# Performance work log

Hardware: AMD Instinct MI355X
Metric: run time of the kernel (lower is better)

## Reference

```python
import jax, jax.numpy as jnp
import numpy as np

N_NODES = 100000
N_EDGES = 1200000
D_FEAT = 64


def setup_inputs() -> dict:
    key = jax.random.key(0)
    k1, k2, k3 = jax.random.split(key, 3)
    x = jax.random.normal(k1, (N_NODES, D_FEAT), dtype=jnp.float32)
    edge_index = jax.random.randint(k2, (2, N_EDGES), 0, N_NODES, dtype=jnp.int64)
    edge_weight = jax.random.uniform(k3, (N_EDGES, 1), dtype=jnp.float32)
    return {"x": x, "edge_index": edge_index, "edge_weight": edge_weight}


def reference(x, edge_index, edge_weight):
    # flow = source_to_target: j = edge_index[0] (source), i = edge_index[1] (target)
    src, dst = edge_index[0], edge_index[1]
    # message: x_j  (gather along node_dim=-2)
    msg = x[src]                       # [E, D]
    # aggregate: scatter-'sum' with edge_weight scaling
    msg = msg * edge_weight            # [E, D]
    out = jax.ops.segment_sum(msg, dst, num_segments=N_NODES)  # [N, D]
    # update: identity
    return out
```

## Files before the change

### kernel.cpp

```cpp
#include <hip/hip_runtime.h>
#include <hip/hip_bf16.h>


constexpr int D_FEAT        = 64;
constexpr int BIN_SHIFT     = 7;
constexpr int NODES_PER_BIN = 1 << BIN_SHIFT;
constexpr int NBINS_MAX     = 1024;
constexpr int BIN_CAP       = 2048;
constexpr int EPB           = 4096;
constexpr int OVF_CAP       = 32768;
constexpr int NKEYS         = 1024;

__device__ __forceinline__ int wave_incl_scan(int v, int lane) {
    #pragma unroll
    for (int d = 1; d < 64; d <<= 1) {
        int t = __shfl_up(v, d);
        if (lane >= d) v += t;
    }
    return v;
}

__device__ __forceinline__ unsigned short f32_to_bf16_rn(float f) {
    unsigned int u = __float_as_uint(f);
    u += 0x7FFFu + ((u >> 16) & 1u);
    return (unsigned short)(u >> 16);
}

__global__ __launch_bounds__(1024) void mp_partition(
    const int* __restrict__ src, const int* __restrict__ dst,
    const float* __restrict__ w, const float* __restrict__ x,
    ushort* __restrict__ xb, int n4,
    int*  __restrict__ gcnt,
    int2* __restrict__ payload,
    int*  __restrict__ ovf_cnt, int4* __restrict__ ovf,
    int n_edges, int nbins)
{
    __shared__ int cnt[NBINS_MAX];
    __shared__ int start[NBINS_MAX];
    __shared__ int cur[NBINS_MAX];
    __shared__ int gbase[NBINS_MAX];
    __shared__ unsigned short binof[EPB];
    __shared__ int2 sorted[EPB];
    __shared__ int wsum[16];

    const int t    = threadIdx.x;
    const int lane = t & 63;
    const int wid  = t >> 6;
    const int base = blockIdx.x * EPB;
    const int nblk = min(EPB, n_edges - base);

    if (t < NBINS_MAX) cnt[t] = 0;

    const int i4 = (base >> 2) + t;
    const bool have = (i4 * 4 < n_edges);
    int4 d4 = make_int4(0, 0, 0, 0);
    if (have) d4 = reinterpret_cast<const int4*>(dst)[i4];

    for (int i = blockIdx.x * 1024 + t; i < n4; i += gridDim.x * 1024) {
        const float4 v = reinterpret_cast<const float4*>(x)[i];
        ushort4 o;
        o.x = f32_to_bf16_rn(v.x);
        o.y = f32_to_bf16_rn(v.y);
        o.z = f32_to_bf16_rn(v.z);
        o.w = f32_to_bf16_rn(v.w);
        reinterpret_cast<ushort4*>(xb)[i] = o;
    }
    __syncthreads();

    if (have) {
        atomicAdd(&cnt[d4.x >> BIN_SHIFT], 1);
        atomicAdd(&cnt[d4.y >> BIN_SHIFT], 1);
        atomicAdd(&cnt[d4.z >> BIN_SHIFT], 1);
        atomicAdd(&cnt[d4.w >> BIN_SHIFT], 1);
    }
    __syncthreads();

    const int c = (t < nbins) ? cnt[t] : 0;
    const int incl = wave_incl_scan(c, lane);
    if (lane == 63) wsum[wid] = incl;
    __syncthreads();
    int woff = 0;
    #pragma unroll
    for (int k = 0; k < 16; ++k) woff += (k < wid) ? wsum[k] : 0;
    const int excl = woff + incl - c;
    if (t < nbins) {
        start[t] = excl;
        cur[t]   = excl;
        if (c > 0) gbase[t] = atomicAdd(&gcnt[t], c);
    }
    __syncthreads();

    if (have) {
        const int4   s4 = reinterpret_cast<const int4*>(src)[i4];
        const float4 w4 = reinterpret_cast<const float4*>(w)[i4];
        const int   dd[4] = {d4.x, d4.y, d4.z, d4.w};
        const int   ss[4] = {s4.x, s4.y, s4.z, s4.w};
        const float ww[4] = {w4.x, w4.y, w4.z, w4.w};
        #pragma unroll
        for (int j = 0; j < 4; ++j) {
            const int b   = dd[j] >> BIN_SHIFT;
            const int low = dd[j] & (NODES_PER_BIN - 1);
            const int p   = atomicAdd(&cur[b], 1);
            sorted[p] = make_int2((low << 20) | ss[j], __float_as_int(ww[j]));
            binof[p]  = (unsigned short)b;
        }
    }
    __syncthreads();

    #pragma unroll
    for (int k = 0; k < EPB / 1024; ++k) {
        const int i = k * 1024 + t;
        if (i >= nblk) break;
        const int b    = binof[i];
        const int idx  = i - start[b];
        const int gpos = gbase[b] + idx;
        const int2 e   = sorted[i];
        if (gpos < BIN_CAP) {
            payload[(size_t)b * BIN_CAP + gpos] = e;
        } else {
            const int op = atomicAdd(ovf_cnt, 1);
            if (op < OVF_CAP)
                ovf[op] = make_int4((b << BIN_SHIFT) + (e.x >> 20),
                                    e.x & 0xFFFFF, e.y, 0);
        }
    }
}


#define ACC8(XV, WW) do {                                          \
    a0 = fmaf(__uint_as_float((XV).x << 16),         (WW), a0);    \
    a1 = fmaf(__uint_as_float((XV).x & 0xFFFF0000u), (WW), a1);    \
    a2 = fmaf(__uint_as_float((XV).y << 16),         (WW), a2);    \
    a3 = fmaf(__uint_as_float((XV).y & 0xFFFF0000u), (WW), a3);    \
    a4 = fmaf(__uint_as_float((XV).z << 16),         (WW), a4);    \
    a5 = fmaf(__uint_as_float((XV).z & 0xFFFF0000u), (WW), a5);    \
    a6 = fmaf(__uint_as_float((XV).w << 16),         (WW), a6);    \
    a7 = fmaf(__uint_as_float((XV).w & 0xFFFF0000u), (WW), a7);    \
} while (0)

__global__ __launch_bounds__(512) void mp_bin_gather(
    const ushort* __restrict__ xb,
    const float*  __restrict__ x,
    const int*  __restrict__ gcnt,
    const int2* __restrict__ payload,
    const int*  __restrict__ ovf_cnt, const int4* __restrict__ ovf,
    float* __restrict__ out, int n_nodes)
{
    __shared__ int2 sraw[BIN_CAP];
    __shared__ int2 sedge[BIN_CAP];
    __shared__ int ncnt[NKEYS];
    __shared__ int nstart[NKEYS + 1];
    __shared__ int ncur[NKEYS];
    __shared__ int wsum[8];

    const int b    = blockIdx.x;
    const int t    = threadIdx.x;
    const int wid  = t >> 6;
    const int lane = t & 63;
    const int sub  = lane >> 3;
    const int fq   = lane & 7;
    const int fg   = fq * 8;

    const int m = min(gcnt[b], BIN_CAP);
    const int2* pl = payload + (size_t)b * BIN_CAP;

    for (int i = t; i < NKEYS; i += 512) ncnt[i] = 0;
    __syncthreads();

    for (int i = t; i < m; i += 512) {
        const int2 e = pl[i];
        sraw[i] = e;
        const int key = ((e.x >> 20) << 3) | ((e.x & 0xFFFFF) >> 14);
        atomicAdd(&ncnt[key], 1);
    }
    __syncthreads();

    {
        const int base0 = wid * 128;
        const int c0 = ncnt[base0 + lane];
        const int c1 = ncnt[base0 + 64 + lane];
        const int s0_ = wave_incl_scan(c0, lane);
        const int t0  = __shfl(s0_, 63);
        const int s1_ = wave_incl_scan(c1, lane) + t0;
        if (lane == 63) wsum[wid] = s1_;
        __syncthreads();
        int cpre = 0;
        #pragma unroll
        for (int k = 0; k < 8; ++k) cpre += (k < wid) ? wsum[k] : 0;
        const int e0 = cpre + s0_ - c0;
        const int e1 = cpre + s1_ - c1;
        nstart[base0 + lane]      = e0;  ncur[base0 + lane]      = e0;
        nstart[base0 + 64 + lane] = e1;  ncur[base0 + 64 + lane] = e1;
        if (t == 511) nstart[NKEYS] = cpre + s1_;
    }
    __syncthreads();

    for (int i = t; i < m; i += 512) {
        const int2 e = sraw[i];
        const int key = ((e.x >> 20) << 3) | ((e.x & 0xFFFFF) >> 14);
        const int p  = atomicAdd(&ncur[key], 1);
        sedge[p] = e;
    }
    __syncthreads();

    const int novf = *ovf_cnt;

    #define XROW(SRC) (*reinterpret_cast<const uint4*>(xb + (size_t)(SRC) * D_FEAT + fg))

    #pragma unroll
    for (int nb = 0; nb < 16; nb += 8) {
        const int n    = wid * 16 + nb + sub;
        const int node = (b << BIN_SHIFT) + n;
        const int s0 = nstart[n << 3];
        const int s1 = nstart[(n + 1) << 3];

        float a0 = 0.f, a1 = 0.f, a2 = 0.f, a3 = 0.f;
        float a4 = 0.f, a5 = 0.f, a6 = 0.f, a7 = 0.f;

        int e = s0;
        for (; e + 4 <= s1; e += 4) {
            const int2 pA = sedge[e];
            const int2 pB = sedge[e + 1];
            const int2 pC = sedge[e + 2];
            const int2 pD = sedge[e + 3];
            const uint4 xA = XROW(pA.x & 0xFFFFF);
            const uint4 xB = XROW(pB.x & 0xFFFFF);
            const uint4 xC = XROW(pC.x & 0xFFFFF);
            const uint4 xD = XROW(pD.x & 0xFFFFF);
            const float wA = __int_as_float(pA.y);
            const float wB = __int_as_float(pB.y);
            const float wC = __int_as_float(pC.y);
            const float wD = __int_as_float(pD.y);
            ACC8(xA, wA);
            ACC8(xB, wB);
            ACC8(xC, wC);
            ACC8(xD, wD);
        }
        if (e + 2 <= s1) {
            const int2 pA = sedge[e];
            const int2 pB = sedge[e + 1];
            const uint4 xA = XROW(pA.x & 0xFFFFF);
            const uint4 xB = XROW(pB.x & 0xFFFFF);
            const float wA = __int_as_float(pA.y);
            const float wB = __int_as_float(pB.y);
            ACC8(xA, wA);
            ACC8(xB, wB);
            e += 2;
        }
        if (e < s1) {
            const int2 p = sedge[e];
            const uint4 xv = XROW(p.x & 0xFFFFF);
            const float ww = __int_as_float(p.y);
            ACC8(xv, ww);
        }

        if (node < n_nodes) {
            if (novf > 0) {
                const int lim = min(novf, OVF_CAP);
                for (int j = 0; j < lim; ++j) {
                    const int4 o = ovf[j];
                    if (o.x == node) {
                        const float* xr = x + (size_t)o.y * D_FEAT + fg;
                        const float ww = __int_as_float(o.z);
                        a0 = fmaf(xr[0], ww, a0); a1 = fmaf(xr[1], ww, a1);
                        a2 = fmaf(xr[2], ww, a2); a3 = fmaf(xr[3], ww, a3);
                        a4 = fmaf(xr[4], ww, a4); a5 = fmaf(xr[5], ww, a5);
                        a6 = fmaf(xr[6], ww, a6); a7 = fmaf(xr[7], ww, a7);
                    }
                }
            }
            float* orow = out + (size_t)node * D_FEAT + fg;
            *reinterpret_cast<float4*>(orow)     = make_float4(a0, a1, a2, a3);
            *reinterpret_cast<float4*>(orow + 4) = make_float4(a4, a5, a6, a7);
        }
    }
    #undef XROW
}

__global__ __launch_bounds__(256) void mp_scatter_atomic(
    const float* __restrict__ x, const int* __restrict__ src,
    const int* __restrict__ dst, const float* __restrict__ w,
    float* __restrict__ out, int n_edges)
{
    const int gtid = blockIdx.x * blockDim.x + threadIdx.x;
    const int edge = gtid >> 6;
    const int lane = threadIdx.x & 63;
    if (edge >= n_edges) return;
    const int s = src[edge];
    const int d = dst[edge];
    const float ww = w[edge];
    atomicAdd(&out[(size_t)d * D_FEAT + lane], x[(size_t)s * D_FEAT + lane] * ww);
}

extern "C" void kernel_launch(void* const* d_in, const int* in_sizes, int n_in,
                              void* d_out, int out_size, void* d_ws, size_t ws_size,
                              hipStream_t stream)
{
    const float* x          = (const float*)d_in[0];
    const int*   edge_index = (const int*)d_in[1];
    const float* w          = (const float*)d_in[2];
    float*       out        = (float*)d_out;

    const int n_edges = in_sizes[1] / 2;
    const int n_nodes = in_sizes[0] / D_FEAT;
    const int* src = edge_index;
    const int* dst = edge_index + n_edges;

    const int nbins = (n_nodes + NODES_PER_BIN - 1) >> BIN_SHIFT;

    int*    gcnt    = (int*)d_ws;
    int*    ovf_cnt = gcnt + NBINS_MAX;
    int4*   ovf     = (int4*)(gcnt + NBINS_MAX + 64);
    int2*   payload = (int2*)(ovf + OVF_CAP);
    ushort* xb      = (ushort*)(payload + (size_t)nbins * BIN_CAP);
    const size_t need = (size_t)(NBINS_MAX + 64) * 4 + (size_t)OVF_CAP * 16
                      + (size_t)nbins * BIN_CAP * 8
                      + (size_t)n_nodes * D_FEAT * 2;

    const bool ok = (ws_size >= need) && (nbins <= NBINS_MAX) && ((n_edges & 3) == 0)
                 && ((n_nodes * D_FEAT) % 4 == 0) && (n_nodes <= 131072);

    if (ok) {
        hipMemsetAsync(gcnt, 0, (size_t)(NBINS_MAX + 64) * 4, stream);
        const int n4 = n_nodes * D_FEAT / 4;
        const int g1 = (n_edges + EPB - 1) / EPB;
        mp_partition<<<g1, 1024, 0, stream>>>(src, dst, w, x, xb, n4,
                                              gcnt, payload, ovf_cnt, ovf,
                                              n_edges, nbins);
        mp_bin_gather<<<nbins, 512, 0, stream>>>(xb, x, gcnt, payload,
                                                 ovf_cnt, ovf, out, n_nodes);
        return;
    }

    hipMemsetAsync(d_out, 0, (size_t)out_size * sizeof(float), stream);
    const int grid = (int)(((size_t)n_edges * 64 + 255) / 256);
    mp_scatter_atomic<<<grid, 256, 0, stream>>>(x, src, dst, w, out, n_edges);
}
```

Before: 126.0 us.

## Halve bin size to 64 nodes and drop the sub-key sort in gather

Bins shrink from 128 to 64 destination nodes, which doubles the bin count to 1563 and halves per-bin capacity. The partition kernel gets a two-element-per-thread scan over 2048 bins. The gather kernel runs with 256 threads and sorts edges by destination node only, dropping the 8-way source sub-key (source locality) ordering. The goal is more, smaller gather blocks for better occupancy and load balance, plus less sort work. In exchange, the partition kernel does more global atomics per block, and the lost source locality may hurt cache reuse.

```diff
diff --git a/kernel.cpp b/kernel.cpp
--- a/kernel.cpp
+++ b/kernel.cpp
@@ -3,13 +3,12 @@
 
 
 constexpr int D_FEAT        = 64;
-constexpr int BIN_SHIFT     = 7;
+constexpr int BIN_SHIFT     = 6;
 constexpr int NODES_PER_BIN = 1 << BIN_SHIFT;
-constexpr int NBINS_MAX     = 1024;
-constexpr int BIN_CAP       = 2048;
+constexpr int NBINS_MAX     = 2048;
+constexpr int BIN_CAP       = 1024;
 constexpr int EPB           = 4096;
 constexpr int OVF_CAP       = 32768;
-constexpr int NKEYS         = 1024;
 
 __device__ __forceinline__ int wave_incl_scan(int v, int lane) {
     #pragma unroll
@@ -49,7 +48,8 @@
     const int base = blockIdx.x * EPB;
     const int nblk = min(EPB, n_edges - base);
 
-    if (t < NBINS_MAX) cnt[t] = 0;
+    cnt[t] = 0;
+    cnt[t + 1024] = 0;
 
     const int i4 = (base >> 2) + t;
     const bool have = (i4 * 4 < n_edges);
@@ -75,18 +75,28 @@
     }
     __syncthreads();
 
-    const int c = (t < nbins) ? cnt[t] : 0;
-    const int incl = wave_incl_scan(c, lane);
-    if (lane == 63) wsum[wid] = incl;
-    __syncthreads();
-    int woff = 0;
-    #pragma unroll
-    for (int k = 0; k < 16; ++k) woff += (k < wid) ? wsum[k] : 0;
-    const int excl = woff + incl - c;
-    if (t < nbins) {
-        start[t] = excl;
-        cur[t]   = excl;
-        if (c > 0) gbase[t] = atomicAdd(&gcnt[t], c);
+    {
+        const int base0 = wid * 128;
+        const int c0 = cnt[base0 + lane];
+        const int c1 = cnt[base0 + 64 + lane];
+        const int s0_ = wave_incl_scan(c0, lane);
+        const int t0  = __shfl(s0_, 63);
+        const int s1_ = wave_incl_scan(c1, lane) + t0;
+        if (lane == 63) wsum[wid] = s1_;
+
+        for (int k = t; k < nbins; k += 1024) {
+            const int c = cnt[k];
+            if (c > 0) gbase[k] = atomicAdd(&gcnt[k], c);
+        }
+        __syncthreads();
+
+        int cpre = 0;
+        #pragma unroll
+        for (int k = 0; k < 16; ++k) cpre += (k < wid) ? wsum[k] : 0;
+        const int e0 = cpre + s0_ - c0;
+        const int e1 = cpre + s1_ - c1;
+        start[base0 + lane]      = e0;  cur[base0 + lane]      = e0;
+        start[base0 + 64 + lane] = e1;  cur[base0 + 64 + lane] = e1;
     }
     __syncthreads();
 
@@ -138,7 +148,7 @@
     a7 = fmaf(__uint_as_float((XV).w & 0xFFFF0000u), (WW), a7);    \
 } while (0)
 
-__global__ __launch_bounds__(512) void mp_bin_gather(
+__global__ __launch_bounds__(256) void mp_bin_gather(
     const ushort* __restrict__ xb,
     const float*  __restrict__ x,
     const int*  __restrict__ gcnt,
@@ -148,10 +158,9 @@
 {
     __shared__ int2 sraw[BIN_CAP];
     __shared__ int2 sedge[BIN_CAP];
-    __shared__ int ncnt[NKEYS];
-    __shared__ int nstart[NKEYS + 1];
-    __shared__ int ncur[NKEYS];
-    __shared__ int wsum[8];
+    __shared__ int ncnt[NODES_PER_BIN];
+    __shared__ int nstart[NODES_PER_BIN + 1];
+    __shared__ int ncur[NODES_PER_BIN];
 
     const int b    = blockIdx.x;
     const int t    = threadIdx.x;
@@ -164,41 +173,28 @@
     const int m = min(gcnt[b], BIN_CAP);
     const int2* pl = payload + (size_t)b * BIN_CAP;
 
-    for (int i = t; i < NKEYS; i += 512) ncnt[i] = 0;
-    __syncthreads();
-
-    for (int i = t; i < m; i += 512) {
+    if (t < NODES_PER_BIN) ncnt[t] = 0;
+    __syncthreads();
+
+    for (int i = t; i < m; i += 256) {
         const int2 e = pl[i];
         sraw[i] = e;
-        const int key = ((e.x >> 20) << 3) | ((e.x & 0xFFFFF) >> 14);
-        atomicAdd(&ncnt[key], 1);
-    }
-    __syncthreads();
-
-    {
-        const int base0 = wid * 128;
-        const int c0 = ncnt[base0 + lane];
-        const int c1 = ncnt[base0 + 64 + lane];
-        const int s0_ = wave_incl_scan(c0, lane);
-        const int t0  = __shfl(s0_, 63);
-        const int s1_ = wave_incl_scan(c1, lane) + t0;
-        if (lane == 63) wsum[wid] = s1_;
-        __syncthreads();
-        int cpre = 0;
-        #pragma unroll
-        for (int k = 0; k < 8; ++k) cpre += (k < wid) ? wsum[k] : 0;
-        const int e0 = cpre + s0_ - c0;
-        const int e1 = cpre + s1_ - c1;
-        nstart[base0 + lane]      = e0;  ncur[base0 + lane]      = e0;
-        nstart[base0 + 64 + lane] = e1;  ncur[base0 + 64 + lane] = e1;
-        if (t == 511) nstart[NKEYS] = cpre + s1_;
-    }
-    __syncthreads();
-
-    for (int i = t; i < m; i += 512) {
+        atomicAdd(&ncnt[e.x >> 20], 1);
+    }
+    __syncthreads();
+
+    if (t < 64) {
+        const int c0 = ncnt[t];
+        const int s0_ = wave_incl_scan(c0, t);
+        nstart[t] = s0_ - c0;
+        ncur[t]   = s0_ - c0;
+        if (t == 63) nstart[64] = s0_;
+    }
+    __syncthreads();
+
+    for (int i = t; i < m; i += 256) {
         const int2 e = sraw[i];
-        const int key = ((e.x >> 20) << 3) | ((e.x & 0xFFFFF) >> 14);
-        const int p  = atomicAdd(&ncur[key], 1);
+        const int p  = atomicAdd(&ncur[e.x >> 20], 1);
         sedge[p] = e;
     }
     __syncthreads();
@@ -211,8 +207,8 @@
     for (int nb = 0; nb < 16; nb += 8) {
         const int n    = wid * 16 + nb + sub;
         const int node = (b << BIN_SHIFT) + n;
-        const int s0 = nstart[n << 3];
-        const int s1 = nstart[(n + 1) << 3];
+        const int s0 = nstart[n];
+        const int s1 = nstart[n + 1];
 
         float a0 = 0.f, a1 = 0.f, a2 = 0.f, a3 = 0.f;
         float a4 = 0.f, a5 = 0.f, a6 = 0.f, a7 = 0.f;
@@ -327,7 +323,7 @@
         mp_partition<<<g1, 1024, 0, stream>>>(src, dst, w, x, xb, n4,
                                               gcnt, payload, ovf_cnt, ovf,
                                               n_edges, nbins);
-        mp_bin_gather<<<nbins, 512, 0, stream>>>(xb, x, gcnt, payload,
+        mp_bin_gather<<<nbins, 256, 0, stream>>>(xb, x, gcnt, payload,
                                                  ovf_cnt, ovf, out, n_nodes);
         return;
     }
```

After: 125.8 us. About the same (-0.1%).

## Fuse partition and bin-gather into one persistent cooperative kernel

Applied to the files above, without the earlier changes.

Replaces the memset, partition kernel and bin-gather kernel with a single cooperative persistent kernel that zeroes its counters, partitions edge chunks through an atomic work queue, converts x to bf16, then uses a grid sync before gathering per-bin. It also simplifies the per-bin sort to key on node only (128 keys instead of 1024 node/source sub-keys) and halves edges per chunk. The aim is to remove launch overhead and the tail between the two phases. In exchange it pays for grid-wide syncs and limits parallelism to the resident-block count. Dropping the source sub-key may also reduce locality in the x row gathers.

```diff
diff --git a/kernel.cpp b/kernel.cpp
--- a/kernel.cpp
+++ b/kernel.cpp
@@ -1,5 +1,8 @@
 #include <hip/hip_runtime.h>
+#include <hip/hip_cooperative_groups.h>
 #include <hip/hip_bf16.h>
+
+namespace cg = cooperative_groups;
 
 
 constexpr int D_FEAT        = 64;
@@ -7,9 +10,9 @@
 constexpr int NODES_PER_BIN = 1 << BIN_SHIFT;
 constexpr int NBINS_MAX     = 1024;
 constexpr int BIN_CAP       = 2048;
-constexpr int EPB           = 4096;
+constexpr int EPB           = 2048;
 constexpr int OVF_CAP       = 32768;
-constexpr int NKEYS         = 1024;
+constexpr int CONV_TILE     = 2048;
 
 __device__ __forceinline__ int wave_incl_scan(int v, int lane) {
     #pragma unroll
@@ -26,106 +29,23 @@
     return (unsigned short)(u >> 16);
 }
 
-__global__ __launch_bounds__(1024) void mp_partition(
-    const int* __restrict__ src, const int* __restrict__ dst,
-    const float* __restrict__ w, const float* __restrict__ x,
-    ushort* __restrict__ xb, int n4,
-    int*  __restrict__ gcnt,
-    int2* __restrict__ payload,
-    int*  __restrict__ ovf_cnt, int4* __restrict__ ovf,
-    int n_edges, int nbins)
-{
-    __shared__ int cnt[NBINS_MAX];
-    __shared__ int start[NBINS_MAX];
-    __shared__ int cur[NBINS_MAX];
-    __shared__ int gbase[NBINS_MAX];
-    __shared__ unsigned short binof[EPB];
-    __shared__ int2 sorted[EPB];
-    __shared__ int wsum[16];
-
-    const int t    = threadIdx.x;
-    const int lane = t & 63;
-    const int wid  = t >> 6;
-    const int base = blockIdx.x * EPB;
-    const int nblk = min(EPB, n_edges - base);
-
-    if (t < NBINS_MAX) cnt[t] = 0;
-
-    const int i4 = (base >> 2) + t;
-    const bool have = (i4 * 4 < n_edges);
-    int4 d4 = make_int4(0, 0, 0, 0);
-    if (have) d4 = reinterpret_cast<const int4*>(dst)[i4];
-
-    for (int i = blockIdx.x * 1024 + t; i < n4; i += gridDim.x * 1024) {
-        const float4 v = reinterpret_cast<const float4*>(x)[i];
-        ushort4 o;
-        o.x = f32_to_bf16_rn(v.x);
-        o.y = f32_to_bf16_rn(v.y);
-        o.z = f32_to_bf16_rn(v.z);
-        o.w = f32_to_bf16_rn(v.w);
-        reinterpret_cast<ushort4*>(xb)[i] = o;
-    }
-    __syncthreads();
-
-    if (have) {
-        atomicAdd(&cnt[d4.x >> BIN_SHIFT], 1);
-        atomicAdd(&cnt[d4.y >> BIN_SHIFT], 1);
-        atomicAdd(&cnt[d4.z >> BIN_SHIFT], 1);
-        atomicAdd(&cnt[d4.w >> BIN_SHIFT], 1);
-    }
-    __syncthreads();
-
-    const int c = (t < nbins) ? cnt[t] : 0;
-    const int incl = wave_incl_scan(c, lane);
-    if (lane == 63) wsum[wid] = incl;
-    __syncthreads();
-    int woff = 0;
-    #pragma unroll
-    for (int k = 0; k < 16; ++k) woff += (k < wid) ? wsum[k] : 0;
-    const int excl = woff + incl - c;
-    if (t < nbins) {
-        start[t] = excl;
-        cur[t]   = excl;
-        if (c > 0) gbase[t] = atomicAdd(&gcnt[t], c);
-    }
-    __syncthreads();
-
-    if (have) {
-        const int4   s4 = reinterpret_cast<const int4*>(src)[i4];
-        const float4 w4 = reinterpret_cast<const float4*>(w)[i4];
-        const int   dd[4] = {d4.x, d4.y, d4.z, d4.w};
-        const int   ss[4] = {s4.x, s4.y, s4.z, s4.w};
-        const float ww[4] = {w4.x, w4.y, w4.z, w4.w};
-        #pragma unroll
-        for (int j = 0; j < 4; ++j) {
-            const int b   = dd[j] >> BIN_SHIFT;
-            const int low = dd[j] & (NODES_PER_BIN - 1);
-            const int p   = atomicAdd(&cur[b], 1);
-            sorted[p] = make_int2((low << 20) | ss[j], __float_as_int(ww[j]));
-            binof[p]  = (unsigned short)b;
-        }
-    }
-    __syncthreads();
-
-    #pragma unroll
-    for (int k = 0; k < EPB / 1024; ++k) {
-        const int i = k * 1024 + t;
-        if (i >= nblk) break;
-        const int b    = binof[i];
-        const int idx  = i - start[b];
-        const int gpos = gbase[b] + idx;
-        const int2 e   = sorted[i];
-        if (gpos < BIN_CAP) {
-            payload[(size_t)b * BIN_CAP + gpos] = e;
-        } else {
-            const int op = atomicAdd(ovf_cnt, 1);
-            if (op < OVF_CAP)
-                ovf[op] = make_int4((b << BIN_SHIFT) + (e.x >> 20),
-                                    e.x & 0xFFFFF, e.y, 0);
-        }
-    }
-}
-
+union SMemU {
+    struct {
+        int cnt[NBINS_MAX];
+        int start[NBINS_MAX];
+        int cur[NBINS_MAX];
+        int gbase[NBINS_MAX];
+        unsigned short binof[EPB];
+        int2 sorted[EPB];
+    } a;
+    struct {
+        int2 sraw[BIN_CAP];
+        int2 sedge[BIN_CAP];
+        int ncnt[NODES_PER_BIN];
+        int nstart[NODES_PER_BIN + 1];
+        int ncur[NODES_PER_BIN];
+    } b;
+};
 
 #define ACC8(XV, WW) do {                                          \
     a0 = fmaf(__uint_as_float((XV).x << 16),         (WW), a0);    \
@@ -138,141 +58,250 @@
     a7 = fmaf(__uint_as_float((XV).w & 0xFFFF0000u), (WW), a7);    \
 } while (0)
 
-__global__ __launch_bounds__(512) void mp_bin_gather(
-    const ushort* __restrict__ xb,
-    const float*  __restrict__ x,
-    const int*  __restrict__ gcnt,
-    const int2* __restrict__ payload,
-    const int*  __restrict__ ovf_cnt, const int4* __restrict__ ovf,
-    float* __restrict__ out, int n_nodes)
+__global__ __launch_bounds__(512) void mp_fused(
+    const int* __restrict__ src, const int* __restrict__ dst,
+    const float* __restrict__ w, const float* __restrict__ x,
+    ushort* __restrict__ xb, int n4,
+    int* __restrict__ gcnt, int2* __restrict__ payload,
+    int* __restrict__ misc, int4* __restrict__ ovf,
+    float* __restrict__ out,
+    int n_edges, int n_nodes, int nbins, int nchunks, int nconv)
 {
-    __shared__ int2 sraw[BIN_CAP];
-    __shared__ int2 sedge[BIN_CAP];
-    __shared__ int ncnt[NKEYS];
-    __shared__ int nstart[NKEYS + 1];
-    __shared__ int ncur[NKEYS];
+    __shared__ SMemU sm;
     __shared__ int wsum[8];
-
-    const int b    = blockIdx.x;
+    __shared__ int sc;
+
     const int t    = threadIdx.x;
     const int wid  = t >> 6;
     const int lane = t & 63;
-    const int sub  = lane >> 3;
-    const int fq   = lane & 7;
-    const int fg   = fq * 8;
-
-    const int m = min(gcnt[b], BIN_CAP);
-    const int2* pl = payload + (size_t)b * BIN_CAP;
-
-    for (int i = t; i < NKEYS; i += 512) ncnt[i] = 0;
-    __syncthreads();
-
-    for (int i = t; i < m; i += 512) {
-        const int2 e = pl[i];
-        sraw[i] = e;
-        const int key = ((e.x >> 20) << 3) | ((e.x & 0xFFFFF) >> 14);
-        atomicAdd(&ncnt[key], 1);
-    }
-    __syncthreads();
-
-    {
-        const int base0 = wid * 128;
-        const int c0 = ncnt[base0 + lane];
-        const int c1 = ncnt[base0 + 64 + lane];
-        const int s0_ = wave_incl_scan(c0, lane);
-        const int t0  = __shfl(s0_, 63);
-        const int s1_ = wave_incl_scan(c1, lane) + t0;
-        if (lane == 63) wsum[wid] = s1_;
-        __syncthreads();
-        int cpre = 0;
+    const int bid  = blockIdx.x;
+    const int gsz  = gridDim.x;
+
+    for (int i = bid * 512 + t; i < NBINS_MAX + 64; i += gsz * 512) {
+        if (i < NBINS_MAX) gcnt[i] = 0;
+        else misc[i - NBINS_MAX] = 0;
+    }
+    cg::this_grid().sync();
+
+    for (;;) {
+        if (t == 0) sc = atomicAdd(&misc[0], 1);
+        __syncthreads();
+        const int c = sc;
+        __syncthreads();
+        if (c >= nchunks) break;
+
+        sm.a.cnt[t]       = 0;
+        sm.a.cnt[t + 512] = 0;
+
+        const int base = c * EPB;
+        const int nblk = min(EPB, n_edges - base);
+        const int i4   = (base >> 2) + t;
+        const bool have = (i4 * 4 < n_edges);
+        int4 d4 = make_int4(0, 0, 0, 0);
+        if (have) d4 = reinterpret_cast<const int4*>(dst)[i4];
+        __syncthreads();
+
+        if (have) {
+            atomicAdd(&sm.a.cnt[d4.x >> BIN_SHIFT], 1);
+            atomicAdd(&sm.a.cnt[d4.y >> BIN_SHIFT], 1);
+            atomicAdd(&sm.a.cnt[d4.z >> BIN_SHIFT], 1);
+            atomicAdd(&sm.a.cnt[d4.w >> BIN_SHIFT], 1);
+        }
+        __syncthreads();
+
+        {
+            const int b0 = wid * 128;
+            const int c0 = sm.a.cnt[b0 + lane];
+            const int c1 = sm.a.cnt[b0 + 64 + lane];
+            const int s0_ = wave_incl_scan(c0, lane);
+            const int t0  = __shfl(s0_, 63);
+            const int s1_ = wave_incl_scan(c1, lane) + t0;
+            if (lane == 63) wsum[wid] = s1_;
+            __syncthreads();
+            int cpre = 0;
+            #pragma unroll
+            for (int k = 0; k < 8; ++k) cpre += (k < wid) ? wsum[k] : 0;
+            const int e0 = cpre + s0_ - c0;
+            const int e1 = cpre + s1_ - c1;
+            sm.a.start[b0 + lane]      = e0;  sm.a.cur[b0 + lane]      = e0;
+            sm.a.start[b0 + 64 + lane] = e1;  sm.a.cur[b0 + 64 + lane] = e1;
+        }
+        for (int k = t; k < nbins; k += 512) {
+            const int cc = sm.a.cnt[k];
+            if (cc > 0) sm.a.gbase[k] = atomicAdd(&gcnt[k], cc);
+        }
+        __syncthreads();
+
+        if (have) {
+            const int4   s4 = reinterpret_cast<const int4*>(src)[i4];
+            const float4 w4 = reinterpret_cast<const float4*>(w)[i4];
+            const int   dd[4] = {d4.x, d4.y, d4.z, d4.w};
+            const int   ss[4] = {s4.x, s4.y, s4.z, s4.w};
+            const float ww[4] = {w4.x, w4.y, w4.z, w4.w};
+            #pragma unroll
+            for (int j = 0; j < 4; ++j) {
+                const int b   = dd[j] >> BIN_SHIFT;
+                const int low = dd[j] & (NODES_PER_BIN - 1);
+                const int p   = atomicAdd(&sm.a.cur[b], 1);
+                sm.a.sorted[p] = make_int2((low << 20) | ss[j], __float_as_int(ww[j]));
+                sm.a.binof[p]  = (unsigned short)b;
+            }
+        }
+        __syncthreads();
+
         #pragma unroll
-        for (int k = 0; k < 8; ++k) cpre += (k < wid) ? wsum[k] : 0;
-        const int e0 = cpre + s0_ - c0;
-        const int e1 = cpre + s1_ - c1;
-        nstart[base0 + lane]      = e0;  ncur[base0 + lane]      = e0;
-        nstart[base0 + 64 + lane] = e1;  ncur[base0 + 64 + lane] = e1;
-        if (t == 511) nstart[NKEYS] = cpre + s1_;
-    }
-    __syncthreads();
-
-    for (int i = t; i < m; i += 512) {
-        const int2 e = sraw[i];
-        const int key = ((e.x >> 20) << 3) | ((e.x & 0xFFFFF) >> 14);
-        const int p  = atomicAdd(&ncur[key], 1);
-        sedge[p] = e;
-    }
-    __syncthreads();
-
-    const int novf = *ovf_cnt;
+        for (int k = 0; k < EPB / 512; ++k) {
+            const int i = k * 512 + t;
+            if (i >= nblk) break;
+            const int b    = sm.a.binof[i];
+            const int idx  = i - sm.a.start[b];
+            const int gpos = sm.a.gbase[b] + idx;
+            const int2 e   = sm.a.sorted[i];
+            if (gpos < BIN_CAP) {
+                payload[(size_t)b * BIN_CAP + gpos] = e;
+            } else {
+                const int op = atomicAdd(&misc[32], 1);
+                if (op < OVF_CAP)
+                    ovf[op] = make_int4((b << BIN_SHIFT) + (e.x >> 20),
+                                        e.x & 0xFFFFF, e.y, 0);
+            }
+        }
+        __syncthreads();
+    }
+
+    for (;;) {
+        if (t == 0) sc = atomicAdd(&misc[16], 1);
+        __syncthreads();
+        const int tile = sc;
+        __syncthreads();
+        if (tile >= nconv) break;
+        const int i0 = tile * CONV_TILE;
+        #pragma unroll
+        for (int k = 0; k < CONV_TILE / 512; ++k) {
+            const int i = i0 + k * 512 + t;
+            if (i < n4) {
+                const float4 v = reinterpret_cast<const float4*>(x)[i];
+                ushort4 o;
+                o.x = f32_to_bf16_rn(v.x);
+                o.y = f32_to_bf16_rn(v.y);
+                o.z = f32_to_bf16_rn(v.z);
+                o.w = f32_to_bf16_rn(v.w);
+                reinterpret_cast<ushort4*>(xb)[i] = o;
+            }
+        }
+    }
+
+    cg::this_grid().sync();
+
+    const int sub = lane >> 3;
+    const int fq  = lane & 7;
+    const int fg  = fq * 8;
+    const int novf = misc[32];
 
     #define XROW(SRC) (*reinterpret_cast<const uint4*>(xb + (size_t)(SRC) * D_FEAT + fg))
 
-    #pragma unroll
-    for (int nb = 0; nb < 16; nb += 8) {
-        const int n    = wid * 16 + nb + sub;
-        const int node = (b << BIN_SHIFT) + n;
-        const int s0 = nstart[n << 3];
-        const int s1 = nstart[(n + 1) << 3];
-
-        float a0 = 0.f, a1 = 0.f, a2 = 0.f, a3 = 0.f;
-        float a4 = 0.f, a5 = 0.f, a6 = 0.f, a7 = 0.f;
-
-        int e = s0;
-        for (; e + 4 <= s1; e += 4) {
-            const int2 pA = sedge[e];
-            const int2 pB = sedge[e + 1];
-            const int2 pC = sedge[e + 2];
-            const int2 pD = sedge[e + 3];
-            const uint4 xA = XROW(pA.x & 0xFFFFF);
-            const uint4 xB = XROW(pB.x & 0xFFFFF);
-            const uint4 xC = XROW(pC.x & 0xFFFFF);
-            const uint4 xD = XROW(pD.x & 0xFFFFF);
-            const float wA = __int_as_float(pA.y);
-            const float wB = __int_as_float(pB.y);
-            const float wC = __int_as_float(pC.y);
-            const float wD = __int_as_float(pD.y);
-            ACC8(xA, wA);
-            ACC8(xB, wB);
-            ACC8(xC, wC);
-            ACC8(xD, wD);
-        }
-        if (e + 2 <= s1) {
-            const int2 pA = sedge[e];
-            const int2 pB = sedge[e + 1];
-            const uint4 xA = XROW(pA.x & 0xFFFFF);
-            const uint4 xB = XROW(pB.x & 0xFFFFF);
-            const float wA = __int_as_float(pA.y);
-            const float wB = __int_as_float(pB.y);
-            ACC8(xA, wA);
-            ACC8(xB, wB);
-            e += 2;
-        }
-        if (e < s1) {
-            const int2 p = sedge[e];
-            const uint4 xv = XROW(p.x & 0xFFFFF);
-            const float ww = __int_as_float(p.y);
-            ACC8(xv, ww);
-        }
-
-        if (node < n_nodes) {
-            if (novf > 0) {
-                const int lim = min(novf, OVF_CAP);
-                for (int j = 0; j < lim; ++j) {
-                    const int4 o = ovf[j];
-                    if (o.x == node) {
-                        const float* xr = x + (size_t)o.y * D_FEAT + fg;
-                        const float ww = __int_as_float(o.z);
-                        a0 = fmaf(xr[0], ww, a0); a1 = fmaf(xr[1], ww, a1);
-                        a2 = fmaf(xr[2], ww, a2); a3 = fmaf(xr[3], ww, a3);
-                        a4 = fmaf(xr[4], ww, a4); a5 = fmaf(xr[5], ww, a5);
-                        a6 = fmaf(xr[6], ww, a6); a7 = fmaf(xr[7], ww, a7);
+    for (int b = bid; b < nbins; b += gsz) {
+        const int m = min(gcnt[b], BIN_CAP);
+        const int2* pl = payload + (size_t)b * BIN_CAP;
+
+        if (t < NODES_PER_BIN) sm.b.ncnt[t] = 0;
+        __syncthreads();
+
+        for (int i = t; i < m; i += 512) {
+            const int2 e = pl[i];
+            sm.b.sraw[i] = e;
+            atomicAdd(&sm.b.ncnt[e.x >> 20], 1);
+        }
+        __syncthreads();
+
+        if (t < 64) {
+            const int c0 = sm.b.ncnt[t], c1 = sm.b.ncnt[64 + t];
+            const int s0_ = wave_incl_scan(c0, t);
+            const int s1_ = wave_incl_scan(c1, t);
+            const int tot0 = __shfl(s0_, 63);
+            const int e0 = s0_ - c0;
+            const int e1 = tot0 + s1_ - c1;
+            sm.b.nstart[t]      = e0;  sm.b.ncur[t]      = e0;
+            sm.b.nstart[64 + t] = e1;  sm.b.ncur[64 + t] = e1;
+            if (t == 63) sm.b.nstart[128] = tot0 + s1_;
+        }
+        __syncthreads();
+
+        for (int i = t; i < m; i += 512) {
+            const int2 e = sm.b.sraw[i];
+            const int p  = atomicAdd(&sm.b.ncur[e.x >> 20], 1);
+            sm.b.sedge[p] = e;
+        }
+        __syncthreads();
+
+        #pragma unroll
+        for (int nb = 0; nb < 16; nb += 8) {
+            const int n    = wid * 16 + nb + sub;
+            const int node = (b << BIN_SHIFT) + n;
+            const int s0 = sm.b.nstart[n];
+            const int s1 = sm.b.nstart[n + 1];
+
+            float a0 = 0.f, a1 = 0.f, a2 = 0.f, a3 = 0.f;
+            float a4 = 0.f, a5 = 0.f, a6 = 0.f, a7 = 0.f;
+
+            int e = s0;
+            for (; e + 4 <= s1; e += 4) {
+                const int2 pA = sm.b.sedge[e];
+                const int2 pB = sm.b.sedge[e + 1];
+                const int2 pC = sm.b.sedge[e + 2];
+                const int2 pD = sm.b.sedge[e + 3];
+                const uint4 xA = XROW(pA.x & 0xFFFFF);
+                const uint4 xB = XROW(pB.x & 0xFFFFF);
+                const uint4 xC = XROW(pC.x & 0xFFFFF);
+                const uint4 xD = XROW(pD.x & 0xFFFFF);
+                const float wA = __int_as_float(pA.y);
+                const float wB = __int_as_float(pB.y);
+                const float wC = __int_as_float(pC.y);
+                const float wD = __int_as_float(pD.y);
+                ACC8(xA, wA);
+                ACC8(xB, wB);
+                ACC8(xC, wC);
+                ACC8(xD, wD);
+            }
+            if (e + 2 <= s1) {
+                const int2 pA = sm.b.sedge[e];
+                const int2 pB = sm.b.sedge[e + 1];
+                const uint4 xA = XROW(pA.x & 0xFFFFF);
+                const uint4 xB = XROW(pB.x & 0xFFFFF);
+                const float wA = __int_as_float(pA.y);
+                const float wB = __int_as_float(pB.y);
+                ACC8(xA, wA);
+                ACC8(xB, wB);
+                e += 2;
+            }
+            if (e < s1) {
+                const int2 p = sm.b.sedge[e];
+                const uint4 xv = XROW(p.x & 0xFFFFF);
+                const float ww = __int_as_float(p.y);
+                ACC8(xv, ww);
+            }
+
+            if (node < n_nodes) {
+                if (novf > 0) {
+                    const int lim = min(novf, OVF_CAP);
+                    for (int j = 0; j < lim; ++j) {
+                        const int4 o = ovf[j];
+                        if (o.x == node) {
+                            const float* xr = x + (size_t)o.y * D_FEAT + fg;
+                            const float ww = __int_as_float(o.z);
+                            a0 = fmaf(xr[0], ww, a0); a1 = fmaf(xr[1], ww, a1);
+                            a2 = fmaf(xr[2], ww, a2); a3 = fmaf(xr[3], ww, a3);
+                            a4 = fmaf(xr[4], ww, a4); a5 = fmaf(xr[5], ww, a5);
+                            a6 = fmaf(xr[6], ww, a6); a7 = fmaf(xr[7], ww, a7);
+                        }
                     }
                 }
-            }
-            float* orow = out + (size_t)node * D_FEAT + fg;
-            *reinterpret_cast<float4*>(orow)     = make_float4(a0, a1, a2, a3);
-            *reinterpret_cast<float4*>(orow + 4) = make_float4(a4, a5, a6, a7);
-        }
+                float* orow = out + (size_t)node * D_FEAT + fg;
+                *reinterpret_cast<float4*>(orow)     = make_float4(a0, a1, a2, a3);
+                *reinterpret_cast<float4*>(orow + 4) = make_float4(a4, a5, a6, a7);
+            }
+        }
+        __syncthreads();
     }
     #undef XROW
 }
@@ -306,10 +335,13 @@
     const int* src = edge_index;
     const int* dst = edge_index + n_edges;
 
-    const int nbins = (n_nodes + NODES_PER_BIN - 1) >> BIN_SHIFT;
+    const int nbins   = (n_nodes + NODES_PER_BIN - 1) >> BIN_SHIFT;
+    const int nchunks = (n_edges + EPB - 1) / EPB;
+    const int n4      = n_nodes * (D_FEAT / 4);
+    const int nconv   = (n4 + CONV_TILE - 1) / CONV_TILE;
 
     int*    gcnt    = (int*)d_ws;
-    int*    ovf_cnt = gcnt + NBINS_MAX;
+    int*    misc    = gcnt + NBINS_MAX;
     int4*   ovf     = (int4*)(gcnt + NBINS_MAX + 64);
     int2*   payload = (int2*)(ovf + OVF_CAP);
     ushort* xb      = (ushort*)(payload + (size_t)nbins * BIN_CAP);
@@ -317,18 +349,38 @@
                       + (size_t)nbins * BIN_CAP * 8
                       + (size_t)n_nodes * D_FEAT * 2;
 
+    static int s_grid = -1;
+    if (s_grid < 0) {
+        hipDeviceProp_t prop;
+        if (hipGetDeviceProperties(&prop, 0) == hipSuccess) {
+            int bpc = 0;
+            if (hipOccupancyMaxActiveBlocksPerMultiprocessor(&bpc, mp_fused, 512, 0)
+                    == hipSuccess && bpc > 0)
+                s_grid = bpc * prop.multiProcessorCount;
+            else
+                s_grid = 0;
+        } else {
+            s_grid = 0;
+        }
+    }
+
     const bool ok = (ws_size >= need) && (nbins <= NBINS_MAX) && ((n_edges & 3) == 0)
-                 && ((n_nodes * D_FEAT) % 4 == 0) && (n_nodes <= 131072);
+                 && ((n_nodes * D_FEAT) % 4 == 0) && (n_nodes <= 131072)
+                 && (s_grid > 0);
 
     if (ok) {
-        hipMemsetAsync(gcnt, 0, (size_t)(NBINS_MAX + 64) * 4, stream);
-        const int n4 = n_nodes * D_FEAT / 4;
-        const int g1 = (n_edges + EPB - 1) / EPB;
-        mp_partition<<<g1, 1024, 0, stream>>>(src, dst, w, x, xb, n4,
-                                              gcnt, payload, ovf_cnt, ovf,
-                                              n_edges, nbins);
-        mp_bin_gather<<<nbins, 512, 0, stream>>>(xb, x, gcnt, payload,
-                                                 ovf_cnt, ovf, out, n_nodes);
+        int grid = s_grid;
+        if (grid > 2048) grid = 2048;
+        void* args[] = {
+            (void*)&src, (void*)&dst, (void*)&w, (void*)&x,
+            (void*)&xb, (void*)&n4,
+            (void*)&gcnt, (void*)&payload, (void*)&misc, (void*)&ovf,
+            (void*)&out,
+            (void*)&n_edges, (void*)&n_nodes, (void*)&nbins,
+            (void*)&nchunks, (void*)&nconv
+        };
+        hipLaunchCooperativeKernel((void*)mp_fused, dim3(grid), dim3(512),
+                                   args, 0, stream);
         return;
     }
 
```

New measurement: 199.6 us. +58.5%, slower.
